# Performance work log

Hardware: AMD Instinct MI355X
Metric: run time of the kernel (lower is better)

Reference implementation:

```python
import jax, jax.numpy as jnp
import numpy as np

D_MODEL = 2048
NUM_HEADS = 16
HEAD_DIM = D_MODEL // NUM_HEADS
B, T = 4, 2048


def setup_inputs() -> dict:
    key = jax.random.key(0)
    ks = jax.random.split(key, 9)
    s = 1.0 / np.sqrt(D_MODEL)
    inp = {"x": jax.random.normal(ks[0], (B, T, D_MODEL), dtype=jnp.float32)}
    for i, name in enumerate(["q", "k", "v", "o"]):
        inp[f"W{name}"] = jax.random.uniform(ks[1 + 2 * i], (D_MODEL, D_MODEL), minval=-s, maxval=s, dtype=jnp.float32)
        inp[f"b{name}"] = jax.random.uniform(ks[2 + 2 * i], (D_MODEL,), minval=-s, maxval=s, dtype=jnp.float32)
    return inp


def reference(x, Wq, bq, Wk, bk, Wv, bv, Wo, bo):
    Bx, Tx, _ = x.shape
    H, Dh = NUM_HEADS, HEAD_DIM
    # torch Linear: y = x @ W.T + b
    q = (x @ Wq.T + bq).reshape(Bx, Tx, H, Dh).transpose(0, 2, 1, 3)  # [B,H,T,D]
    k = (x @ Wk.T + bk).reshape(Bx, Tx, H, Dh).transpose(0, 2, 1, 3)
    v = (x @ Wv.T + bv).reshape(Bx, Tx, H, Dh).transpose(0, 2, 1, 3)
    scale = 1.0 / np.sqrt(Dh).astype(np.float32)
    scores = jnp.einsum('bhqd,bhkd->bhqk', q, k) * scale  # [B,H,T,T] (no causal mask, as in source)
    attn = jax.nn.softmax(scores, axis=-1)
    out = jnp.einsum('bhqk,bhkd->bhqd', attn, v)  # [B,H,T,D]
    out = out.transpose(0, 2, 1, 3).reshape(Bx, Tx, H * Dh)
    return out @ Wo.T + bo
```

## Files before the change

### kernel.cpp

```cpp
#include <hip/hip_runtime.h>
#include <hip/hip_bf16.h>

typedef __bf16 bf16x8 __attribute__((ext_vector_type(8)));
typedef __bf16 bf16x4 __attribute__((ext_vector_type(4)));
typedef float floatx4 __attribute__((ext_vector_type(4)));

#define MFMA16(a, b, c) __builtin_amdgcn_mfma_f32_16x16x32_bf16((a), (b), (c), 0, 0, 0)

#define GLOAD16(g, l) __builtin_amdgcn_global_load_lds( \
    (const __attribute__((address_space(1))) unsigned int*)(g), \
    (__attribute__((address_space(3))) unsigned int*)(l), 16, 0, 0)

static constexpr int DM = 2048, NH = 16, HD = 128, BATCH = 4, SEQ = 2048;
static constexpr int MROWS = BATCH * SEQ;
static constexpr float SCALE = 0.08838834764831845f;
static constexpr float PMAX = 3.0f;

static constexpr size_t XE = (size_t)MROWS * DM;
static constexpr size_t WE = (size_t)DM * DM;

__global__ __launch_bounds__(256) void cvt_all(
    const float* __restrict__ x, const float* __restrict__ Wq,
    const float* __restrict__ Wk, const float* __restrict__ Wv,
    const float* __restrict__ Wo, __bf16* __restrict__ dst) {
  const size_t total = XE + 4 * WE;
  size_t stride = (size_t)gridDim.x * 256 * 8;
  for (size_t i = ((size_t)blockIdx.x * 256 + threadIdx.x) * 8; i < total; i += stride) {
    const float* src;
    size_t off;
    if (i < XE) { src = x; off = i; }
    else {
      size_t j = i - XE;
      int seg = (int)(j / WE);
      off = j - (size_t)seg * WE;
      src = seg == 0 ? Wq : (seg == 1 ? Wk : (seg == 2 ? Wv : Wo));
    }
    float4 a = *reinterpret_cast<const float4*>(src + off);
    float4 b = *reinterpret_cast<const float4*>(src + off + 4);
    bf16x8 r;
    r[0] = (__bf16)a.x; r[1] = (__bf16)a.y; r[2] = (__bf16)a.z; r[3] = (__bf16)a.w;
    r[4] = (__bf16)b.x; r[5] = (__bf16)b.y; r[6] = (__bf16)b.z; r[7] = (__bf16)b.w;
    *reinterpret_cast<bf16x8*>(dst + i) = r;
  }
}

__device__ __forceinline__ void gemm256_core(
    const __bf16* __restrict__ A, const __bf16* __restrict__ W,
    unsigned short* sA, unsigned short* sB,
    int tm, int tn, floatx4 (&acc)[8][4]) {
  const int tid = threadIdx.x;
  const int wave = tid >> 6, lane = tid & 63;
  const int q = lane >> 4, ml = lane & 15;
  const int wm = wave >> 2, wn = wave & 3;

  const int csrc = (tid & 3) ^ ((tid >> 3) & 3);
  const __bf16* gA = A + (size_t)(tm + (tid >> 2)) * DM + csrc * 8;
  const __bf16* gB = W + (size_t)(tn + (tid >> 2)) * DM + csrc * 8;
  const size_t rstep = (size_t)128 * DM;
  const int ldsW = wave * 512;

  const int fsw = (q ^ ((ml >> 1) & 3)) * 8;
  const int aOff = (wm * 128 + ml) * 32 + fsw;
  const int bOff = (wn * 64 + ml) * 32 + fsw;

#define STAGE256(s_) do { \
    const int _r = ((s_) & 3) * 8192;   \
    const int _k = (s_) * 32;           \
    GLOAD16(gA + _k,         sA + _r + ldsW); \
    GLOAD16(gA + _k + rstep, sA + _r + 4096 + ldsW); \
    GLOAD16(gB + _k,         sB + _r + ldsW); \
    GLOAD16(gB + _k + rstep, sB + _r + 4096 + ldsW); \
  } while (0)

#define GPHASE(p_, vm_, stage_) do { \
    if (stage_) STAGE256((p_) + 3); \
    asm volatile("s_waitcnt vmcnt(%0)" :: "i"(vm_) : "memory"); \
    __builtin_amdgcn_s_barrier(); \
    __builtin_amdgcn_sched_barrier(0); \
    const int regO = ((p_) & 3) * 8192; \
    bf16x8 aF[8], bF[4]; \
    _Pragma("unroll") \
    for (int t = 0; t < 4; ++t) \
      bF[t] = *reinterpret_cast<const bf16x8*>(sB + regO + bOff + t * 512); \
    _Pragma("unroll") \
    for (int t = 0; t < 8; ++t) \
      aF[t] = *reinterpret_cast<const bf16x8*>(sA + regO + aOff + t * 512); \
    __builtin_amdgcn_s_setprio(1); \
    _Pragma("unroll") \
    for (int mt = 0; mt < 8; ++mt) \
      _Pragma("unroll") \
      for (int ct = 0; ct < 4; ++ct) \
        acc[mt][ct] = MFMA16(aF[mt], bF[ct], acc[mt][ct]); \
    __builtin_amdgcn_s_setprio(0); \
    __builtin_amdgcn_s_barrier(); \
  } while (0)

  STAGE256(0); STAGE256(1); STAGE256(2);

#pragma unroll 4
  for (int p = 0; p < 60; ++p) GPHASE(p, 12, 1);
  GPHASE(60, 12, 1);
  GPHASE(61, 8, 0);
  GPHASE(62, 4, 0);
  GPHASE(63, 0, 0);
#undef GPHASE
#undef STAGE256
}

__global__ __launch_bounds__(512, 2) void qkv_gemm256(
    const __bf16* __restrict__ X,
    const __bf16* __restrict__ Wq, const __bf16* __restrict__ Wk,
    const __bf16* __restrict__ Wv,
    const float* __restrict__ bq, const float* __restrict__ bk,
    const float* __restrict__ bv,
    __bf16* __restrict__ qh, __bf16* __restrict__ kh, __bf16* __restrict__ vt) {
  __shared__ unsigned short sA[4 * 256 * 32];
  __shared__ unsigned short sB[4 * 256 * 32];
  const int bx = blockIdx.x;
  const int which = bx >> 3;
  const int tn = (bx & 7) * 256;
  const int tm = blockIdx.y * 256;
  const __bf16* W = which == 0 ? Wq : (which == 1 ? Wk : Wv);
  const float* bias = which == 0 ? bq : (which == 1 ? bk : bv);

  floatx4 acc[8][4] = {};
  gemm256_core(X, W, sA, sB, tm, tn, acc);

  const int tid = threadIdx.x, wave = tid >> 6, lane = tid & 63;
  const int q = lane >> 4, ml = lane & 15;
  const int wm = wave >> 2, wn = wave & 3;

  __syncthreads();

  if (which < 2) {
    unsigned short* reg = (wave < 4) ? sA + wave * 8192 : sB + (wave - 4) * 8192;
#pragma unroll
    for (int ct = 0; ct < 4; ++ct) {
      int n = tn + wn * 64 + ct * 16 + ml;
      float bv_ = bias[n];
#pragma unroll
      for (int mt = 0; mt < 8; ++mt)
#pragma unroll
        for (int r = 0; r < 4; ++r) {
          int row = mt * 16 + q * 4 + r;
          int col = ct * 16 + ml;
          __bf16 pb = (__bf16)(acc[mt][ct][r] + bv_);
          reg[row * 64 + (((col >> 3) ^ ((row >> 1) & 7)) << 3) + (col & 7)] =
              __builtin_bit_cast(unsigned short, pb);
        }
    }
    __bf16* dst = which == 0 ? qh : kh;
    const int rr = lane >> 3, cc = lane & 7;
#pragma unroll
    for (int i = 0; i < 16; ++i) {
      int row = i * 8 + rr;
      int4 v = *reinterpret_cast<const int4*>(
          reg + row * 64 + ((cc ^ ((row >> 1) & 7)) << 3));
      int m = tm + wm * 128 + row;
      int n0 = tn + wn * 64 + cc * 8;
      int b = m >> 11, t = m & 2047, h = n0 >> 7, d = n0 & 127;
      *reinterpret_cast<int4*>(dst + ((size_t)(b * 16 + h) * SEQ + t) * HD + d) = v;
    }
  } else {
#pragma unroll
    for (int ct = 0; ct < 4; ++ct) {
      int n = tn + wn * 64 + ct * 16 + ml;
      float bv_ = bias[n];
      int h = n >> 7, d = n & 127;
#pragma unroll
      for (int mt = 0; mt < 8; ++mt) {
        int m0 = tm + wm * 128 + mt * 16 + q * 4;
        int b = m0 >> 11, t = m0 & 2047;
        bf16x4 pk;
#pragma unroll
        for (int r = 0; r < 4; ++r) pk[r] = (__bf16)(acc[mt][ct][r] + bv_);
        *reinterpret_cast<bf16x4*>(vt + (size_t)((b * 16 + h) * 128 + d) * SEQ + t) = pk;
      }
    }
  }
}

__global__ __launch_bounds__(512, 2) void proj_gemm256(
    const __bf16* __restrict__ A, const __bf16* __restrict__ W,
    const float* __restrict__ bias, float* __restrict__ out) {
  __shared__ unsigned short sA[4 * 256 * 32];
  __shared__ unsigned short sB[4 * 256 * 32];
  const int tn = blockIdx.x * 256;
  const int tm = blockIdx.y * 256;

  floatx4 acc[8][4] = {};
  gemm256_core(A, W, sA, sB, tm, tn, acc);

  const int tid = threadIdx.x, wave = tid >> 6, lane = tid & 63;
  const int q = lane >> 4, ml = lane & 15;
  const int wm = wave >> 2, wn = wave & 3;
#pragma unroll
  for (int ct = 0; ct < 4; ++ct) {
    int n = tn + wn * 64 + ct * 16 + ml;
    float bv_ = bias[n];
#pragma unroll
    for (int mt = 0; mt < 8; ++mt) {
      int m0 = tm + wm * 128 + mt * 16 + q * 4;
#pragma unroll
      for (int r = 0; r < 4; ++r)
        out[(size_t)(m0 + r) * DM + n] = acc[mt][ct][r] + bv_;
    }
  }
}

__global__ __launch_bounds__(256, 2) void mha_attn(
    const __bf16* __restrict__ Q, const __bf16* __restrict__ Kg,
    const __bf16* __restrict__ Vt, __bf16* __restrict__ O) {
  __shared__ unsigned short sK[2][64 * 128];
  __shared__ unsigned short sV[2][128 * 64];
  __shared__ unsigned short sP[128 * 64];

  const int tid = threadIdx.x;
  const int bh = blockIdx.x;
  const int t0 = blockIdx.y * 128;
  const int wave = tid >> 6, lane = tid & 63;
  const int q = lane >> 4, ml = lane & 15;
  const int wrow = wave * 32;

  bf16x8 qf[2][4];
#pragma unroll
  for (int mt = 0; mt < 2; ++mt) {
    const __bf16* qrow = Q + ((size_t)bh * SEQ + t0 + wrow + mt * 16 + ml) * HD;
#pragma unroll
    for (int s = 0; s < 4; ++s)
      qf[mt][s] = *reinterpret_cast<const bf16x8*>(qrow + s * 32 + q * 8);
  }

  floatx4 oacc[2][8] = {};
  float lsum[2][4] = {};

  const __bf16* kbase = Kg + (size_t)bh * SEQ * HD;
  const __bf16* vbase = Vt + (size_t)bh * HD * SEQ;

#define ASTAGE(slot_, key0_) do { \
    _Pragma("unroll") \
    for (int i = 0; i < 4; ++i) { \
      int krow = i * 16 + (tid >> 4); \
      int kc = (tid & 15) ^ (krow & 7); \
      GLOAD16(kbase + (size_t)((key0_) + krow) * HD + kc * 8, \
              &sK[slot_][i * 2048 + wave * 512]); \
      int vrow = i * 32 + (tid >> 3); \
      int vc = (tid & 7) ^ (vrow & 7); \
      GLOAD16(vbase + (size_t)vrow * SEQ + (key0_) + vc * 8, \
              &sV[slot_][i * 2048 + wave * 512]); \
    } } while (0)

#define ACOMPUTE(S_) do { \
    floatx4 sacc[2][4] = {}; \
    _Pragma("unroll") \
    for (int s = 0; s < 4; ++s) { \
      _Pragma("unroll") \
      for (int ct = 0; ct < 4; ++ct) { \
        bf16x8 kf = *reinterpret_cast<const bf16x8*>( \
            &sK[S_][(ct * 16 + ml) * 128 + (((s * 4 + q) ^ (ml & 7)) * 8)]); \
        sacc[0][ct] = MFMA16(qf[0][s], kf, sacc[0][ct]); \
        sacc[1][ct] = MFMA16(qf[1][s], kf, sacc[1][ct]); \
      } \
    } \
    _Pragma("unroll") \
    for (int mt = 0; mt < 2; ++mt) \
      _Pragma("unroll") \
      for (int ct = 0; ct < 4; ++ct) \
        _Pragma("unroll") \
        for (int r = 0; r < 4; ++r) { \
          float p = __expf(fmaf(sacc[mt][ct][r], SCALE, -PMAX)); \
          lsum[mt][r] += p; \
          __bf16 pb = (__bf16)p; \
          int lr = wrow + mt * 16 + q * 4 + r; \
          int ch = ct * 2 + (ml >> 3); \
          sP[lr * 64 + ((ch ^ (lr & 7)) << 3) + (ml & 7)] = \
              __builtin_bit_cast(unsigned short, pb); \
        } \
    _Pragma("unroll") \
    for (int s = 0; s < 2; ++s) { \
      bf16x8 pf0 = *reinterpret_cast<const bf16x8*>( \
          &sP[(wrow + ml) * 64 + (((s * 4 + q) ^ (ml & 7)) << 3)]); \
      bf16x8 pf1 = *reinterpret_cast<const bf16x8*>( \
          &sP[(wrow + 16 + ml) * 64 + (((s * 4 + q) ^ (ml & 7)) << 3)]); \
      _Pragma("unroll") \
      for (int ot = 0; ot < 8; ++ot) { \
        bf16x8 vf = *reinterpret_cast<const bf16x8*>( \
            &sV[S_][(ot * 16 + ml) * 64 + (((s * 4 + q) ^ (ml & 7)) * 8)]); \
        oacc[0][ot] = MFMA16(pf0, vf, oacc[0][ot]); \
        oacc[1][ot] = MFMA16(pf1, vf, oacc[1][ot]); \
      } \
    } } while (0)

  ASTAGE(0, 0);
  for (int kt = 0; kt < 31; ++kt) {
    const int S = kt & 1;
    ASTAGE(S ^ 1, (kt + 1) * 64);
    asm volatile("s_waitcnt vmcnt(8)" ::: "memory");
    __builtin_amdgcn_s_barrier();
    __builtin_amdgcn_sched_barrier(0);
    __builtin_amdgcn_s_setprio(1);
    ACOMPUTE(S);
    __builtin_amdgcn_s_setprio(0);
    asm volatile("" ::: "memory");
    __builtin_amdgcn_s_barrier();
  }
  asm volatile("s_waitcnt vmcnt(0)" ::: "memory");
  __builtin_amdgcn_s_barrier();
  __builtin_amdgcn_sched_barrier(0);
  ACOMPUTE(1);
#undef ACOMPUTE
#undef ASTAGE

#pragma unroll
  for (int mt = 0; mt < 2; ++mt)
#pragma unroll
    for (int r = 0; r < 4; ++r) {
      float s = lsum[mt][r];
      s += __shfl_xor(s, 1); s += __shfl_xor(s, 2);
      s += __shfl_xor(s, 4); s += __shfl_xor(s, 8);
      lsum[mt][r] = 1.0f / s;
    }

  const int b = bh >> 4, h = bh & 15;
  const int rr = lane >> 3, cc = lane & 7;
  __bf16* obase = O + ((size_t)b * SEQ + t0 + wrow) * DM + h * HD;
#pragma unroll
  for (int pass = 0; pass < 2; ++pass) {
    __builtin_amdgcn_sched_barrier(0);
#pragma unroll
    for (int mt = 0; mt < 2; ++mt)
#pragma unroll
      for (int ot = 0; ot < 4; ++ot)
#pragma unroll
        for (int r = 0; r < 4; ++r) {
          int lr = wrow + mt * 16 + q * 4 + r;
          int ch = ot * 2 + (ml >> 3);
          __bf16 ob = (__bf16)(oacc[mt][pass * 4 + ot][r] * lsum[mt][r]);
          sP[lr * 64 + ((ch ^ (lr & 7)) << 3) + (ml & 7)] =
              __builtin_bit_cast(unsigned short, ob);
        }
#pragma unroll
    for (int i = 0; i < 4; ++i) {
      int row32 = i * 8 + rr;
      int gr = wrow + row32;
      int4 v = *reinterpret_cast<const int4*>(
          &sP[gr * 64 + ((cc ^ (gr & 7)) << 3)]);
      *reinterpret_cast<int4*>(obase + (size_t)row32 * DM + pass * 64 + cc * 8) = v;
    }
  }
}

__device__ inline bf16x8 ld8s(const float* p) {
  float4 a = *reinterpret_cast<const float4*>(p);
  float4 b = *reinterpret_cast<const float4*>(p + 4);
  bf16x8 r;
  r[0] = (__bf16)a.x; r[1] = (__bf16)a.y; r[2] = (__bf16)a.z; r[3] = (__bf16)a.w;
  r[4] = (__bf16)b.x; r[5] = (__bf16)b.y; r[6] = (__bf16)b.z; r[7] = (__bf16)b.w;
  return r;
}
__device__ inline bf16x8 ld8s(const __bf16* p) {
  int4 v = *reinterpret_cast<const int4*>(p);
  return __builtin_bit_cast(bf16x8, v);
}

template <typename TA>
__global__ __launch_bounds__(256) void gemm_slow(
    const TA* __restrict__ A, const float* __restrict__ W,
    const float* __restrict__ bias, void* __restrict__ C, int mode, int out_f32) {
  __shared__ unsigned short sA[128 * 72];
  __shared__ unsigned short sW[128 * 72];
  const int tid = threadIdx.x;
  const int tn = blockIdx.x * 128, tm = blockIdx.y * 128;
  const int wave = tid >> 6, lane = tid & 63;
  const int q = lane >> 4, ml = lane & 15;
  const int waveM = (wave >> 1) * 64, waveN = (wave & 1) * 64;
  const int srow = tid >> 3, sc8 = tid & 7;
  floatx4 acc[4][4] = {};
  for (int k0 = 0; k0 < DM; k0 += 64) {
    bf16x8 va[4], vb[4];
#pragma unroll
    for (int i = 0; i < 4; ++i) {
      int row = srow + 32 * i;
      va[i] = ld8s(A + (size_t)(tm + row) * DM + k0 + sc8 * 8);
      vb[i] = ld8s(W + (size_t)(tn + row) * DM + k0 + sc8 * 8);
    }
    __syncthreads();
#pragma unroll
    for (int i = 0; i < 4; ++i) {
      int row = srow + 32 * i;
      *reinterpret_cast<int4*>(&sA[row * 72 + sc8 * 8]) = __builtin_bit_cast(int4, va[i]);
      *reinterpret_cast<int4*>(&sW[row * 72 + sc8 * 8]) = __builtin_bit_cast(int4, vb[i]);
    }
    __syncthreads();
#pragma unroll
    for (int s = 0; s < 2; ++s) {
      bf16x8 aF[4], bF[4];
#pragma unroll
      for (int t = 0; t < 4; ++t)
        aF[t] = *reinterpret_cast<const bf16x8*>(&sA[(waveM + t * 16 + ml) * 72 + s * 32 + q * 8]);
#pragma unroll
      for (int t = 0; t < 4; ++t)
        bF[t] = *reinterpret_cast<const bf16x8*>(&sW[(waveN + t * 16 + ml) * 72 + s * 32 + q * 8]);
#pragma unroll
      for (int rt = 0; rt < 4; ++rt)
#pragma unroll
        for (int ct = 0; ct < 4; ++ct)
          acc[rt][ct] = MFMA16(aF[rt], bF[ct], acc[rt][ct]);
    }
  }
#pragma unroll
  for (int ct = 0; ct < 4; ++ct) {
    int n = tn + waveN + ct * 16 + ml;
    float bv = bias[n];
    int h = n >> 7, d = n & 127;
#pragma unroll
    for (int rt = 0; rt < 4; ++rt) {
      int m0 = tm + waveM + rt * 16 + q * 4;
      int b = m0 >> 11, t = m0 & 2047;
      if (mode == 0) {
        if (out_f32) {
#pragma unroll
          for (int r = 0; r < 4; ++r)
            ((float*)C)[(size_t)(m0 + r) * DM + n] = acc[rt][ct][r] + bv;
        } else {
#pragma unroll
          for (int r = 0; r < 4; ++r)
            ((__bf16*)C)[(size_t)(m0 + r) * DM + n] = (__bf16)(acc[rt][ct][r] + bv);
        }
      } else if (mode == 1) {
        bf16x4 pk;
#pragma unroll
        for (int r = 0; r < 4; ++r) pk[r] = (__bf16)(acc[rt][ct][r] + bv);
        *reinterpret_cast<bf16x4*>((__bf16*)C + (size_t)((b * 16 + h) * 128 + d) * SEQ + t) = pk;
      } else {
#pragma unroll
        for (int r = 0; r < 4; ++r)
          ((__bf16*)C)[((size_t)(b * 16 + h) * SEQ + t + r) * HD + d] =
              (__bf16)(acc[rt][ct][r] + bv);
      }
    }
  }
}

extern "C" void kernel_launch(void* const* d_in, const int* in_sizes, int n_in,
                              void* d_out, int out_size, void* d_ws, size_t ws_size,
                              hipStream_t stream) {
  const float* x  = (const float*)d_in[0];
  const float* Wq = (const float*)d_in[1]; const float* bq = (const float*)d_in[2];
  const float* Wk = (const float*)d_in[3]; const float* bk = (const float*)d_in[4];
  const float* Wv = (const float*)d_in[5]; const float* bv = (const float*)d_in[6];
  const float* Wo = (const float*)d_in[7]; const float* bo = (const float*)d_in[8];

  const size_t needA = 64 + 2 * (4 * XE + 4 * WE);
  dim3 gq(24, 32), gp(8, 32), gs(16, 64), ga(BATCH * NH, SEQ / 128);

  if (ws_size >= needA + 256) {
    __bf16* xc  = (__bf16*)((char*)d_ws + 64);
    __bf16* Wqc = xc + XE;
    __bf16* Wkc = Wqc + WE;
    __bf16* Wvc = Wkc + WE;
    __bf16* Woc = Wvc + WE;
    __bf16* qh  = Woc + WE;
    __bf16* kh  = qh + XE;
    __bf16* vt  = kh + XE;
    __bf16* aw  = xc;

    cvt_all<<<4096, 256, 0, stream>>>(x, Wq, Wk, Wv, Wo, xc);
    qkv_gemm256<<<gq, 512, 0, stream>>>(xc, Wqc, Wkc, Wvc, bq, bk, bv, qh, kh, vt);
    mha_attn<<<ga, 256, 0, stream>>>(qh, kh, vt, aw);
    proj_gemm256<<<gp, 512, 0, stream>>>(aw, Woc, bo, (float*)d_out);
  } else {
    __bf16* qh = (__bf16*)((char*)d_ws + 64);
    __bf16* kh = qh + XE;
    __bf16* vt = kh + XE;
    __bf16* aw = vt + XE;
    gemm_slow<float><<<gs, 256, 0, stream>>>(x, Wq, bq, qh, 2, 0);
    gemm_slow<float><<<gs, 256, 0, stream>>>(x, Wk, bk, kh, 2, 0);
    gemm_slow<float><<<gs, 256, 0, stream>>>(x, Wv, bv, vt, 1, 0);
    mha_attn<<<ga, 256, 0, stream>>>(qh, kh, vt, aw);
    gemm_slow<__bf16><<<gs, 256, 0, stream>>>(aw, Wo, bo, d_out, 0, 1);
  }
}
```

Measured before the change: 613.0 us.

## Keep softmax probabilities in registers and double attention block to 512 threads

```diff
diff --git a/kernel.cpp b/kernel.cpp
--- a/kernel.cpp
+++ b/kernel.cpp
@@ -208,16 +208,14 @@
   }
 }
 
-__global__ __launch_bounds__(256, 2) void mha_attn(
+__global__ __launch_bounds__(512, 2) void mha_attn(
     const __bf16* __restrict__ Q, const __bf16* __restrict__ Kg,
     const __bf16* __restrict__ Vt, __bf16* __restrict__ O) {
-  __shared__ unsigned short sK[2][64 * 128];
-  __shared__ unsigned short sV[2][128 * 64];
-  __shared__ unsigned short sP[128 * 64];
+  __shared__ unsigned short smem[32768];
 
   const int tid = threadIdx.x;
   const int bh = blockIdx.x;
-  const int t0 = blockIdx.y * 128;
+  const int t0 = blockIdx.y * 256;
   const int wave = tid >> 6, lane = tid & 63;
   const int q = lane >> 4, ml = lane & 15;
   const int wrow = wave * 32;
@@ -232,62 +230,67 @@
   }
 
   floatx4 oacc[2][8] = {};
-  float lsum[2][4] = {};
+  float lsum0 = 0.f, lsum1 = 0.f;
 
   const __bf16* kbase = Kg + (size_t)bh * SEQ * HD;
   const __bf16* vbase = Vt + (size_t)bh * HD * SEQ;
 
-#define ASTAGE(slot_, key0_) do { \
-    _Pragma("unroll") \
-    for (int i = 0; i < 4; ++i) { \
-      int krow = i * 16 + (tid >> 4); \
+#define ASTAGE(S_, key0_) do { \
+    _Pragma("unroll") \
+    for (int i = 0; i < 2; ++i) { \
+      int krow = i * 32 + (tid >> 4); \
       int kc = (tid & 15) ^ (krow & 7); \
       GLOAD16(kbase + (size_t)((key0_) + krow) * HD + kc * 8, \
-              &sK[slot_][i * 2048 + wave * 512]); \
-      int vrow = i * 32 + (tid >> 3); \
+              smem + (S_) * 8192 + i * 4096 + wave * 512); \
+      int vrow = i * 64 + (tid >> 3); \
       int vc = (tid & 7) ^ (vrow & 7); \
       GLOAD16(vbase + (size_t)vrow * SEQ + (key0_) + vc * 8, \
-              &sV[slot_][i * 2048 + wave * 512]); \
+              smem + 16384 + (S_) * 8192 + i * 4096 + wave * 512); \
     } } while (0)
 
 #define ACOMPUTE(S_) do { \
+    const unsigned short* K_ = smem + (S_) * 8192; \
+    const unsigned short* V_ = smem + 16384 + (S_) * 8192; \
     floatx4 sacc[2][4] = {}; \
     _Pragma("unroll") \
     for (int s = 0; s < 4; ++s) { \
       _Pragma("unroll") \
       for (int ct = 0; ct < 4; ++ct) { \
         bf16x8 kf = *reinterpret_cast<const bf16x8*>( \
-            &sK[S_][(ct * 16 + ml) * 128 + (((s * 4 + q) ^ (ml & 7)) * 8)]); \
-        sacc[0][ct] = MFMA16(qf[0][s], kf, sacc[0][ct]); \
-        sacc[1][ct] = MFMA16(qf[1][s], kf, sacc[1][ct]); \
+            &K_[(ct * 16 + ml) * 128 + (((s * 4 + q) ^ (ml & 7)) * 8)]); \
+        sacc[0][ct] = MFMA16(kf, qf[0][s], sacc[0][ct]); \
+        sacc[1][ct] = MFMA16(kf, qf[1][s], sacc[1][ct]); \
       } \
     } \
     _Pragma("unroll") \
-    for (int mt = 0; mt < 2; ++mt) \
+    for (int ct = 0; ct < 4; ++ct) \
       _Pragma("unroll") \
-      for (int ct = 0; ct < 4; ++ct) \
-        _Pragma("unroll") \
-        for (int r = 0; r < 4; ++r) { \
-          float p = __expf(fmaf(sacc[mt][ct][r], SCALE, -PMAX)); \
-          lsum[mt][r] += p; \
-          __bf16 pb = (__bf16)p; \
-          int lr = wrow + mt * 16 + q * 4 + r; \
-          int ch = ct * 2 + (ml >> 3); \
-          sP[lr * 64 + ((ch ^ (lr & 7)) << 3) + (ml & 7)] = \
-              __builtin_bit_cast(unsigned short, pb); \
-        } \
+      for (int r = 0; r < 4; ++r) { \
+        float p0 = __expf(fmaf(sacc[0][ct][r], SCALE, -PMAX)); \
+        float p1 = __expf(fmaf(sacc[1][ct][r], SCALE, -PMAX)); \
+        lsum0 += p0; lsum1 += p1; \
+        sacc[0][ct][r] = p0; sacc[1][ct][r] = p1; \
+      } \
     _Pragma("unroll") \
     for (int s = 0; s < 2; ++s) { \
-      bf16x8 pf0 = *reinterpret_cast<const bf16x8*>( \
-          &sP[(wrow + ml) * 64 + (((s * 4 + q) ^ (ml & 7)) << 3)]); \
-      bf16x8 pf1 = *reinterpret_cast<const bf16x8*>( \
-          &sP[(wrow + 16 + ml) * 64 + (((s * 4 + q) ^ (ml & 7)) << 3)]); \
+      bf16x8 af0, af1; \
+      _Pragma("unroll") \
+      for (int j = 0; j < 4; ++j) { \
+        af0[j] = (__bf16)sacc[0][2 * s][j];     af0[4 + j] = (__bf16)sacc[0][2 * s + 1][j]; \
+        af1[j] = (__bf16)sacc[1][2 * s][j];     af1[4 + j] = (__bf16)sacc[1][2 * s + 1][j]; \
+      } \
       _Pragma("unroll") \
       for (int ot = 0; ot < 8; ++ot) { \
-        bf16x8 vf = *reinterpret_cast<const bf16x8*>( \
-            &sV[S_][(ot * 16 + ml) * 64 + (((s * 4 + q) ^ (ml & 7)) * 8)]); \
-        oacc[0][ot] = MFMA16(pf0, vf, oacc[0][ot]); \
-        oacc[1][ot] = MFMA16(pf1, vf, oacc[1][ot]); \
+        const int vb = (ot * 16 + ml) * 64; \
+        bf16x4 lo = *reinterpret_cast<const bf16x4*>( \
+            &V_[vb + (((4 * s + (q >> 1)) ^ (ml & 7)) * 8) + 4 * (q & 1)]); \
+        bf16x4 hi = *reinterpret_cast<const bf16x4*>( \
+            &V_[vb + (((4 * s + 2 + (q >> 1)) ^ (ml & 7)) * 8) + 4 * (q & 1)]); \
+        bf16x8 vf; \
+        vf[0] = lo[0]; vf[1] = lo[1]; vf[2] = lo[2]; vf[3] = lo[3]; \
+        vf[4] = hi[0]; vf[5] = hi[1]; vf[6] = hi[2]; vf[7] = hi[3]; \
+        oacc[0][ot] = MFMA16(af0, vf, oacc[0][ot]); \
+        oacc[1][ot] = MFMA16(af1, vf, oacc[1][ot]); \
       } \
     } } while (0)
 
@@ -295,7 +298,7 @@
   for (int kt = 0; kt < 31; ++kt) {
     const int S = kt & 1;
     ASTAGE(S ^ 1, (kt + 1) * 64);
-    asm volatile("s_waitcnt vmcnt(8)" ::: "memory");
+    asm volatile("s_waitcnt vmcnt(4)" ::: "memory");
     __builtin_amdgcn_s_barrier();
     __builtin_amdgcn_sched_barrier(0);
     __builtin_amdgcn_s_setprio(1);
@@ -311,41 +314,40 @@
 #undef ACOMPUTE
 #undef ASTAGE
 
+  lsum0 += __shfl_xor(lsum0, 16); lsum0 += __shfl_xor(lsum0, 32);
+  lsum1 += __shfl_xor(lsum1, 16); lsum1 += __shfl_xor(lsum1, 32);
+  float inv[2][4];
+#pragma unroll
+  for (int r = 0; r < 4; ++r) {
+    inv[0][r] = 1.0f / __shfl(lsum0, q * 4 + r);
+    inv[1][r] = 1.0f / __shfl(lsum1, q * 4 + r);
+  }
+
+  __syncthreads();
+  unsigned short* scr = smem + wave * 4096;
 #pragma unroll
   for (int mt = 0; mt < 2; ++mt)
 #pragma unroll
-    for (int r = 0; r < 4; ++r) {
-      float s = lsum[mt][r];
-      s += __shfl_xor(s, 1); s += __shfl_xor(s, 2);
-      s += __shfl_xor(s, 4); s += __shfl_xor(s, 8);
-      lsum[mt][r] = 1.0f / s;
-    }
-
+    for (int ot = 0; ot < 8; ++ot)
+#pragma unroll
+      for (int r = 0; r < 4; ++r) {
+        int lr = mt * 16 + q * 4 + r;
+        __bf16 ob = (__bf16)(oacc[mt][ot][r] * inv[mt][r]);
+        scr[lr * 128 + ((ot ^ (lr & 7)) * 16) + ml] =
+            __builtin_bit_cast(unsigned short, ob);
+      }
   const int b = bh >> 4, h = bh & 15;
-  const int rr = lane >> 3, cc = lane & 7;
   __bf16* obase = O + ((size_t)b * SEQ + t0 + wrow) * DM + h * HD;
 #pragma unroll
-  for (int pass = 0; pass < 2; ++pass) {
-    __builtin_amdgcn_sched_barrier(0);
-#pragma unroll
-    for (int mt = 0; mt < 2; ++mt)
-#pragma unroll
-      for (int ot = 0; ot < 4; ++ot)
-#pragma unroll
-        for (int r = 0; r < 4; ++r) {
-          int lr = wrow + mt * 16 + q * 4 + r;
-          int ch = ot * 2 + (ml >> 3);
-          __bf16 ob = (__bf16)(oacc[mt][pass * 4 + ot][r] * lsum[mt][r]);
-          sP[lr * 64 + ((ch ^ (lr & 7)) << 3) + (ml & 7)] =
-              __builtin_bit_cast(unsigned short, ob);
-        }
-#pragma unroll
-    for (int i = 0; i < 4; ++i) {
-      int row32 = i * 8 + rr;
-      int gr = wrow + row32;
+  for (int i = 0; i < 4; ++i) {
+    int lr = i * 8 + (lane >> 3);
+#pragma unroll
+    for (int p = 0; p < 2; ++p) {
+      int d0 = p * 64 + (lane & 7) * 8;
+      int chunk = d0 >> 4;
       int4 v = *reinterpret_cast<const int4*>(
-          &sP[gr * 64 + ((cc ^ (gr & 7)) << 3)]);
-      *reinterpret_cast<int4*>(obase + (size_t)row32 * DM + pass * 64 + cc * 8) = v;
+          &scr[lr * 128 + ((chunk ^ (lr & 7)) * 16) + (d0 & 15)]);
+      *reinterpret_cast<int4*>(obase + (size_t)lr * DM + d0) = v;
     }
   }
 }
@@ -452,7 +454,7 @@
   const float* Wo = (const float*)d_in[7]; const float* bo = (const float*)d_in[8];
 
   const size_t needA = 64 + 2 * (4 * XE + 4 * WE);
-  dim3 gq(24, 32), gp(8, 32), gs(16, 64), ga(BATCH * NH, SEQ / 128);
+  dim3 gq(24, 32), gp(8, 32), gs(16, 64), ga(BATCH * NH, SEQ / 256);
 
   if (ws_size >= needA + 256) {
     __bf16* xc  = (__bf16*)((char*)d_ws + 64);
@@ -467,7 +469,7 @@
 
     cvt_all<<<4096, 256, 0, stream>>>(x, Wq, Wk, Wv, Wo, xc);
     qkv_gemm256<<<gq, 512, 0, stream>>>(xc, Wqc, Wkc, Wvc, bq, bk, bv, qh, kh, vt);
-    mha_attn<<<ga, 256, 0, stream>>>(qh, kh, vt, aw);
+    mha_attn<<<ga, 512, 0, stream>>>(qh, kh, vt, aw);
     proj_gemm256<<<gp, 512, 0, stream>>>(aw, Woc, bo, (float*)d_out);
   } else {
     __bf16* qh = (__bf16*)((char*)d_ws + 64);
@@ -477,7 +479,7 @@
     gemm_slow<float><<<gs, 256, 0, stream>>>(x, Wq, bq, qh, 2, 0);
     gemm_slow<float><<<gs, 256, 0, stream>>>(x, Wk, bk, kh, 2, 0);
     gemm_slow<float><<<gs, 256, 0, stream>>>(x, Wv, bv, vt, 1, 0);
-    mha_attn<<<ga, 256, 0, stream>>>(qh, kh, vt, aw);
+    mha_attn<<<ga, 512, 0, stream>>>(qh, kh, vt, aw);
     gemm_slow<__bf16><<<gs, 256, 0, stream>>>(aw, Wo, bo, d_out, 0, 1);
   }
 }
```

After: 603.6 us. Within noise of the previous version (-1.5%).
